# Optimization experiments

Hardware: AMD Instinct MI355X
Metric: run time of the kernel (lower is better)

The kernel has to match this reference:

```python
import jax, jax.numpy as jnp
import numpy as np

NUM_EMBEDDINGS = 1024
EMBEDDING_DIM = 256
COMMITMENT_COST = 0.02


def setup_inputs() -> dict:
    key = jax.random.key(0)
    k1, k2 = jax.random.split(key)
    z = jax.random.normal(k1, (64, 256, 32, 32), dtype=jnp.float32)
    # torch init: uniform(-1/K, 1/K)
    emb = jax.random.uniform(k2, (NUM_EMBEDDINGS, EMBEDDING_DIM), dtype=jnp.float32,
                             minval=-1.0 / NUM_EMBEDDINGS, maxval=1.0 / NUM_EMBEDDINGS)
    return {"z": z, "emb": emb}


def reference(z, emb):
    n, d, h, w = z.shape
    # (N, D, H, W) -> (N*H*W, D)
    z_flat = jnp.transpose(z, (0, 2, 3, 1)).reshape(-1, d)
    # squared L2 distances: ||z||^2 - 2 z.E^T + ||E||^2  -> (NHW, K)
    distances = (jnp.sum(z_flat * z_flat, axis=1, keepdims=True)
                 - 2.0 * z_flat @ emb.T
                 + jnp.sum(emb * emb, axis=1))
    indices = jnp.argmin(distances, axis=1)  # (NHW,)
    z_q = jnp.transpose(emb[indices].reshape(n, h, w, d), (0, 3, 1, 2))  # (N, D, H, W)
    # straight-through estimator
    z_q_st = z + jax.lax.stop_gradient(z_q - z)
    commitment_loss = COMMITMENT_COST * jnp.mean((jax.lax.stop_gradient(z) - z_q) ** 2)
    codebook_loss = jnp.mean((z - jax.lax.stop_gradient(z_q)) ** 2)
    vq_loss = commitment_loss + codebook_loss
    indices_reshaped = indices.reshape(n, h, w)
    return z_q_st, indices_reshaped, vq_loss
```

## Files before the change

### kernel.cpp

```cpp
#include <hip/hip_runtime.h>
#include <hip/hip_bf16.h>
#include <float.h>

#define OUT_IDX_OFF 16777216
#define OUT_LOSS_OFF 16842752
#define CAND_OFF 8388608
#define GMIN_OFF 12582912
#define GCNT_OFF 13107200
#define NSLOT 32
#define DELTA 2.0e-3f

typedef __attribute__((ext_vector_type(8))) short short8;
typedef __attribute__((ext_vector_type(4))) float f32x4;

static __device__ __forceinline__ unsigned short f2bf(float f) {
  union { __hip_bfloat16 h; unsigned short u; } cv;
  cv.h = __float2bfloat16(f);
  return cv.u;
}

__global__ __launch_bounds__(256) void k_prep(const float* __restrict__ emb,
                                              unsigned short* __restrict__ E2,
                                              float* __restrict__ cws) {
  const int k = blockIdx.x, d = threadIdx.x;
  const float v = emb[k * 256 + d];
  __shared__ float red[256];
  __shared__ unsigned short row[256];
  row[d] = f2bf(v);
  red[d] = v * v;
  __syncthreads();
  for (int s = 128; s > 0; s >>= 1) {
    if (d < s) red[d] += red[d + s];
    __syncthreads();
  }
  if (d == 0) cws[k] = red[0];
  if (d < 32) ((short8*)&E2[k * 256])[d] = ((short8*)row)[d];
}

__global__ __launch_bounds__(256) void k_cvt2(const float* __restrict__ z,
                                              unsigned short* __restrict__ A2) {
  __shared__ float tile[64][65];
  const int t = threadIdx.x;
  const int pt = blockIdx.x >> 2, dt = blockIdx.x & 3;
  const int p0 = pt << 6, d0 = dt << 6;
  const int n = p0 >> 10, hw0 = p0 & 1023;
  const float* zb = z + (size_t)n * 262144 + (size_t)d0 * 1024 + hw0;
  const int hwl = (t & 15) << 2;
#pragma unroll
  for (int i = 0; i < 4; ++i) {
    const int dl = (t >> 4) + i * 16;
    const float4 v = *(const float4*)&zb[(size_t)dl * 1024 + hwl];
    tile[hwl + 0][dl] = v.x;
    tile[hwl + 1][dl] = v.y;
    tile[hwl + 2][dl] = v.z;
    tile[hwl + 3][dl] = v.w;
  }
  __syncthreads();
  const int pl = t >> 2, c = t & 3;
  unsigned short* dst = &A2[(size_t)(p0 + pl) * 256 + d0];
#pragma unroll
  for (int h = 0; h < 2; ++h) {
    const int ch = c + h * 4;
    unsigned short tmp[8];
#pragma unroll
    for (int j = 0; j < 8; ++j) tmp[j] = f2bf(tile[pl][ch * 8 + j]);
    *(short8*)&dst[ch * 8] = *(short8*)tmp;
  }
}

__global__ __launch_bounds__(256) void k_a(const float* __restrict__ z,
                                           float* __restrict__ aws) {
#pragma clang fp contract(off)
  const int t = threadIdx.x;
  const int r = (blockIdx.x << 7) + (t & 127);
  const int h = t >> 7;
  const int n = r >> 10;
  const int hw = r & 1023;
  const float* zp = z + (size_t)n * 262144 + hw + (size_t)h * 131072;
  float acc[8];
#pragma unroll
  for (int j = 0; j < 8; ++j) {
    const float x = zp[(size_t)j * 1024];
    acc[j] = x * x;
  }
  for (int g = 1; g < 16; ++g) {
#pragma unroll
    for (int j = 0; j < 8; ++j) {
      const float x = zp[(size_t)(g * 8 + j) * 1024];
      const float p = x * x;
      acc[j] = acc[j] + p;
    }
  }
  const float s = ((acc[0] + acc[1]) + (acc[2] + acc[3])) +
                  ((acc[4] + acc[5]) + (acc[6] + acc[7]));
  __shared__ float red[256];
  red[t] = s;
  __syncthreads();
  if (t < 128) aws[(blockIdx.x << 7) + t] = red[t] + red[t + 128];
}

__global__ __launch_bounds__(256, 4) void k_gemm4(
    const unsigned short* __restrict__ A2, const unsigned short* __restrict__ E2,
    const float* __restrict__ cws, const float* __restrict__ aws,
    int* __restrict__ gmin, int* __restrict__ gcnt,
    float2* __restrict__ gcand) {
  __shared__ __align__(16) unsigned short As[128 * 64];
  __shared__ __align__(16) unsigned short Bs[128 * 64];
  __shared__ float a_l[128], c_l[128], rmkt[256], bmin[128];

  const int t = threadIdx.x;
  const int lane = t & 63;
  const int wave = __builtin_amdgcn_readfirstlane(t >> 6);
  const int wr = wave >> 1, wc = wave & 1;
  const int quad = lane >> 4, l15 = lane & 15;
  const int swa = l15 & 7;

  const int bid = blockIdx.x;
  const int L = ((bid & 7) << 9) + (bid >> 3);
  const int rb = L >> 3, ck = L & 7;
  const int r0 = rb << 7, k0 = ck << 7;

  if (t < 128) {
    a_l[t] = aws[r0 + t];
    c_l[t] = cws[k0 + t];
  }

  const int srow = t >> 3;
  const int gpos = t & 7;

  f32x4 acc[4][4];
#pragma unroll
  for (int a = 0; a < 4; ++a)
#pragma unroll
    for (int b = 0; b < 4; ++b) acc[a][b] = (f32x4)(0.0f);

  for (int kt = 0; kt < 4; ++kt) {
    if (kt) __syncthreads();
#pragma unroll
    for (int i = 0; i < 4; ++i) {
      const int row = (i << 5) + srow;
      const int gsrc = gpos ^ (row & 7);
      const unsigned short* sa =
          A2 + (((size_t)(r0 + row)) << 8) + (kt << 6) + (gsrc << 3);
      __builtin_amdgcn_global_load_lds(
          (const __attribute__((address_space(1))) void*)sa,
          (__attribute__((address_space(3))) void*)(As + (i << 11) +
                                                    (wave << 9)),
          16, 0, 0);
      const unsigned short* sb =
          E2 + (((size_t)(k0 + row)) << 8) + (kt << 6) + (gsrc << 3);
      __builtin_amdgcn_global_load_lds(
          (const __attribute__((address_space(1))) void*)sb,
          (__attribute__((address_space(3))) void*)(Bs + (i << 11) +
                                                    (wave << 9)),
          16, 0, 0);
    }
    __syncthreads();
#pragma unroll
    for (int ks = 0; ks < 2; ++ks) {
      short8 af[4], bf[4];
#pragma unroll
      for (int tr = 0; tr < 4; ++tr)
        af[tr] = *(const short8*)&As[(wr * 64 + tr * 16 + l15) * 64 +
                                     (((ks * 4 + quad) ^ swa) << 3)];
#pragma unroll
      for (int tc = 0; tc < 4; ++tc)
        bf[tc] = *(const short8*)&Bs[(wc * 64 + tc * 16 + l15) * 64 +
                                     (((ks * 4 + quad) ^ swa) << 3)];
#pragma unroll
      for (int tr = 0; tr < 4; ++tr)
#pragma unroll
        for (int tc = 0; tc < 4; ++tc)
          acc[tr][tc] = __builtin_amdgcn_mfma_f32_16x16x32_bf16(
              af[tr], bf[tc], acc[tr][tc], 0, 0, 0);
    }
  }

#pragma unroll
  for (int tr = 0; tr < 4; ++tr)
#pragma unroll
    for (int rg = 0; rg < 4; ++rg) {
      const int rloc = wr * 64 + tr * 16 + quad * 4 + rg;
      const float av = a_l[rloc];
      float mn = FLT_MAX;
#pragma unroll
      for (int tc = 0; tc < 4; ++tc) {
        const int cloc = wc * 64 + tc * 16 + l15;
        const float s = av + fmaf(-2.0f, acc[tr][tc][rg], c_l[cloc]);
        mn = fminf(mn, s);
      }
      mn = fminf(mn, __shfl_xor(mn, 1));
      mn = fminf(mn, __shfl_xor(mn, 2));
      mn = fminf(mn, __shfl_xor(mn, 4));
      mn = fminf(mn, __shfl_xor(mn, 8));
      if (l15 == 0) rmkt[rloc * 2 + wc] = mn;
    }
  __syncthreads();
  if (t < 128) {
    const float m = fminf(rmkt[t * 2], rmkt[t * 2 + 1]);
    const int old = atomicMin(&gmin[r0 + t], __float_as_int(m));
    bmin[t] = fminf(m, __int_as_float(old));
  }
  __syncthreads();
#pragma unroll
  for (int tr = 0; tr < 4; ++tr)
#pragma unroll
    for (int rg = 0; rg < 4; ++rg) {
      const int rloc = wr * 64 + tr * 16 + quad * 4 + rg;
      const float av = a_l[rloc];
      const float lim = bmin[rloc] + DELTA;
#pragma unroll
      for (int tc = 0; tc < 4; ++tc) {
        const int cloc = wc * 64 + tc * 16 + l15;
        const float s = av + fmaf(-2.0f, acc[tr][tc][rg], c_l[cloc]);
        if (s <= lim) {
          const int pos = atomicAdd(&gcnt[r0 + rloc], 1);
          if (pos < NSLOT)
            gcand[(size_t)(r0 + rloc) * NSLOT + pos] =
                make_float2(s, __int_as_float(k0 + cloc));
        }
      }
    }
}

__global__ __launch_bounds__(256) void k_finish(
    const float* __restrict__ z, const float* __restrict__ emb,
    const float* __restrict__ cws, const float* __restrict__ aws,
    const int* __restrict__ gmin, const int* __restrict__ gcnt,
    const float2* __restrict__ gcand, int* __restrict__ idxws,
    float* __restrict__ out) {
  const int tid = (blockIdx.x << 8) + threadIdx.x;
  const int r = tid >> 2, sub = tid & 3;
  const float lim = __int_as_float(gmin[r]) + DELTA;
  int m = gcnt[r];
  if (m > NSLOT) m = NSLOT;
  const int n = r >> 10, hw = r & 1023;
  const float* zp = z + (size_t)n * 262144 + hw;
  const float a = aws[r];
  float bestv = FLT_MAX;
  int besti = 0x7fffffff;
  for (int ci = sub; ci < m; ci += 4) {
    const float2 p = gcand[(size_t)r * NSLOT + ci];
    if (p.x > lim) continue;
    const int k = __float_as_int(p.y);
    const float* ep = emb + (size_t)k * 256;
    float dot = 0.0f;
#pragma unroll 8
    for (int d = 0; d < 256; ++d) dot = fmaf(zp[(size_t)d * 1024], ep[d], dot);
    float s = fmaf(-2.0f, dot, a);
    s = s + cws[k];
    if (s < bestv || (s == bestv && k < besti)) {
      bestv = s;
      besti = k;
    }
  }
#pragma unroll
  for (int off = 1; off < 4; off <<= 1) {
    const float ov = __shfl_xor(bestv, off);
    const int oi = __shfl_xor(besti, off);
    if (ov < bestv || (ov == bestv && oi < besti)) {
      bestv = ov;
      besti = oi;
    }
  }
  if (sub == 0) {
    idxws[r] = besti;
    out[OUT_IDX_OFF + r] = (float)besti;
  }
  float c = (sub == 0) ? bestv : 0.0f;
#pragma unroll
  for (int off = 1; off < 64; off <<= 1) c += __shfl_xor(c, off);
  if ((threadIdx.x & 63) == 0)
    atomicAdd(&out[OUT_LOSS_OFF], c * (1.02f / 16777216.0f));
}

__global__ __launch_bounds__(256) void k_out2(const float* __restrict__ emb,
                                              const int* __restrict__ idxws,
                                              float* __restrict__ out) {
  __shared__ float zq[32][257];
  __shared__ int sidx[32];
  const int t = threadIdx.x;
  const int p0 = blockIdx.x << 5;
  const int n = p0 >> 10, hw0 = p0 & 1023;
  if (t < 32) sidx[t] = idxws[p0 + t];
  __syncthreads();
#pragma unroll
  for (int it = 0; it < 8; ++it) {
    const int i = t + (it << 8);
    const int p = i >> 6;
    const int q = (i & 63) << 2;
    const float4 v = *(const float4*)&emb[(size_t)sidx[p] * 256 + q];
    zq[p][q] = v.x;
    zq[p][q + 1] = v.y;
    zq[p][q + 2] = v.z;
    zq[p][q + 3] = v.w;
  }
  __syncthreads();
  const int p = t & 31, d0 = t >> 5;
  float* ob = out + (size_t)n * 262144 + hw0 + p;
#pragma unroll
  for (int dd = 0; dd < 32; ++dd) {
    const int d = (dd << 3) + d0;
    ob[(size_t)d * 1024] = zq[p][d];
  }
}

extern "C" void kernel_launch(void* const* d_in, const int* in_sizes, int n_in,
                              void* d_out, int out_size, void* d_ws,
                              size_t ws_size, hipStream_t stream) {
  const float* z = (const float*)d_in[0];
  const float* emb = (const float*)d_in[1];
  float* out = (float*)d_out;

  unsigned short* E2 = (unsigned short*)d_ws;
  float* cws = (float*)(E2 + 262144);
  float* aws = cws + 1024;
  int* idxws = (int*)(aws + 65536);
  unsigned short* A2 = (unsigned short*)d_out;
  float2* gcand = (float2*)(out + CAND_OFF);
  int* gmin = (int*)(out + GMIN_OFF);
  int* gcnt = (int*)(out + GCNT_OFF);

  hipMemsetAsync((char*)d_out + (size_t)OUT_LOSS_OFF * 4, 0, 4, stream);
  hipMemsetAsync(gmin, 0x7f, 65536 * 4, stream);
  hipMemsetAsync(gcnt, 0, 65536 * 4, stream);

  k_prep<<<dim3(1024), dim3(256), 0, stream>>>(emb, E2, cws);
  k_cvt2<<<dim3(4096), dim3(256), 0, stream>>>(z, A2);
  k_a<<<dim3(512), dim3(256), 0, stream>>>(z, aws);
  k_gemm4<<<dim3(4096), dim3(256), 0, stream>>>(A2, E2, cws, aws, gmin, gcnt,
                                                gcand);
  k_finish<<<dim3(1024), dim3(256), 0, stream>>>(z, emb, cws, aws, gmin, gcnt,
                                                 gcand, idxws, out);
  k_out2<<<dim3(2048), dim3(256), 0, stream>>>(emb, idxws, out);
}
```

Before: 317.9 us.

## Pre-swizzle operands into MFMA fragment layout and load directly from global

The conversion kernels now write A and E in bf16 into a fragment-ordered layout that matches the MFMA register fragments, so each lane's short8 sits contiguously per wave. The GEMM kernel drops its LDS staging buffers and barriers and reads fragments straight from global memory with coalesced 16-byte loads. This removes the LDS round trip and the per-k-step syncs. The cost is that tiles shared across blocks are no longer reused through LDS, so more traffic goes to L2. Occupancy is lowered to 3 blocks per unit, which gives more registers but can expose global load latency.

```diff
diff --git a/kernel.cpp b/kernel.cpp
--- a/kernel.cpp
+++ b/kernel.cpp
@@ -19,13 +19,14 @@
   return cv.u;
 }
 
+
 __global__ __launch_bounds__(256) void k_prep(const float* __restrict__ emb,
                                               unsigned short* __restrict__ E2,
                                               float* __restrict__ cws) {
   const int k = blockIdx.x, d = threadIdx.x;
   const float v = emb[k * 256 + d];
   __shared__ float red[256];
-  __shared__ unsigned short row[256];
+  __shared__ __align__(16) unsigned short row[256];
   row[d] = f2bf(v);
   red[d] = v * v;
   __syncthreads();
@@ -34,10 +35,17 @@
     __syncthreads();
   }
   if (d == 0) cws[k] = red[0];
-  if (d < 32) ((short8*)&E2[k * 256])[d] = ((short8*)row)[d];
-}
-
-__global__ __launch_bounds__(256) void k_cvt2(const float* __restrict__ z,
+  if (d < 32) {
+    const int kt = d >> 3, ks = (d >> 2) & 1, quad = d & 3;
+    const int ck = k >> 7, wc = (k >> 6) & 1, tc = (k >> 4) & 3, l15 = k & 15;
+    const int slab = ck * 64 + kt * 16 + ks * 8 + wc * 4 + tc;
+    const int d0 = kt * 64 + ks * 32 + quad * 8;
+    *(short8*)&E2[(((size_t)slab << 6) + (quad << 4) + l15) << 3] =
+        *(const short8*)&row[d0];
+  }
+}
+
+__global__ __launch_bounds__(256) void k_cvt3(const float* __restrict__ z,
                                               unsigned short* __restrict__ A2) {
   __shared__ float tile[64][65];
   const int t = threadIdx.x;
@@ -56,15 +64,19 @@
     tile[hwl + 3][dl] = v.w;
   }
   __syncthreads();
-  const int pl = t >> 2, c = t & 3;
-  unsigned short* dst = &A2[(size_t)(p0 + pl) * 256 + d0];
+  const int rb = pt >> 1, wr = pt & 1, kt = dt;
+  const size_t base_sh = ((size_t)(rb * 64 + wr * 32 + kt * 8)) << 9;
 #pragma unroll
   for (int h = 0; h < 2; ++h) {
-    const int ch = c + h * 4;
+    const int o = t + (h << 8);
+    const int l15o = o & 15, quado = (o >> 4) & 3;
+    const int tro = (o >> 6) & 3, kso = o >> 8;
+    const int pl = tro * 16 + l15o;
+    const int dlb = kso * 32 + quado * 8;
     unsigned short tmp[8];
 #pragma unroll
-    for (int j = 0; j < 8; ++j) tmp[j] = f2bf(tile[pl][ch * 8 + j]);
-    *(short8*)&dst[ch * 8] = *(short8*)tmp;
+    for (int j = 0; j < 8; ++j) tmp[j] = f2bf(tile[pl][dlb + j]);
+    *(short8*)&A2[base_sh + ((size_t)o << 3)] = *(short8*)tmp;
   }
 }
 
@@ -99,13 +111,11 @@
   if (t < 128) aws[(blockIdx.x << 7) + t] = red[t] + red[t + 128];
 }
 
-__global__ __launch_bounds__(256, 4) void k_gemm4(
+__global__ __launch_bounds__(256, 3) void k_gemm5(
     const unsigned short* __restrict__ A2, const unsigned short* __restrict__ E2,
     const float* __restrict__ cws, const float* __restrict__ aws,
     int* __restrict__ gmin, int* __restrict__ gcnt,
     float2* __restrict__ gcand) {
-  __shared__ __align__(16) unsigned short As[128 * 64];
-  __shared__ __align__(16) unsigned short Bs[128 * 64];
   __shared__ float a_l[128], c_l[128], rmkt[256], bmin[128];
 
   const int t = threadIdx.x;
@@ -113,7 +123,6 @@
   const int wave = __builtin_amdgcn_readfirstlane(t >> 6);
   const int wr = wave >> 1, wc = wave & 1;
   const int quad = lane >> 4, l15 = lane & 15;
-  const int swa = l15 & 7;
 
   const int bid = blockIdx.x;
   const int L = ((bid & 7) << 9) + (bid >> 3);
@@ -125,8 +134,10 @@
     c_l[t] = cws[k0 + t];
   }
 
-  const int srow = t >> 3;
-  const int gpos = t & 7;
+  const short8* Ab =
+      (const short8*)(A2 + (((((size_t)(rb * 64 + wr * 32)) << 6) + lane) << 3));
+  const short8* Bb =
+      (const short8*)(E2 + (((((size_t)(ck * 64 + wc * 4)) << 6) + lane) << 3));
 
   f32x4 acc[4][4];
 #pragma unroll
@@ -134,39 +145,17 @@
 #pragma unroll
     for (int b = 0; b < 4; ++b) acc[a][b] = (f32x4)(0.0f);
 
+#pragma unroll
   for (int kt = 0; kt < 4; ++kt) {
-    if (kt) __syncthreads();
-#pragma unroll
-    for (int i = 0; i < 4; ++i) {
-      const int row = (i << 5) + srow;
-      const int gsrc = gpos ^ (row & 7);
-      const unsigned short* sa =
-          A2 + (((size_t)(r0 + row)) << 8) + (kt << 6) + (gsrc << 3);
-      __builtin_amdgcn_global_load_lds(
-          (const __attribute__((address_space(1))) void*)sa,
-          (__attribute__((address_space(3))) void*)(As + (i << 11) +
-                                                    (wave << 9)),
-          16, 0, 0);
-      const unsigned short* sb =
-          E2 + (((size_t)(k0 + row)) << 8) + (kt << 6) + (gsrc << 3);
-      __builtin_amdgcn_global_load_lds(
-          (const __attribute__((address_space(1))) void*)sb,
-          (__attribute__((address_space(3))) void*)(Bs + (i << 11) +
-                                                    (wave << 9)),
-          16, 0, 0);
-    }
-    __syncthreads();
 #pragma unroll
     for (int ks = 0; ks < 2; ++ks) {
       short8 af[4], bf[4];
 #pragma unroll
       for (int tr = 0; tr < 4; ++tr)
-        af[tr] = *(const short8*)&As[(wr * 64 + tr * 16 + l15) * 64 +
-                                     (((ks * 4 + quad) ^ swa) << 3)];
+        af[tr] = Ab[(kt * 8 + ks * 4 + tr) * 64];
 #pragma unroll
       for (int tc = 0; tc < 4; ++tc)
-        bf[tc] = *(const short8*)&Bs[(wc * 64 + tc * 16 + l15) * 64 +
-                                     (((ks * 4 + quad) ^ swa) << 3)];
+        bf[tc] = Bb[(kt * 16 + ks * 8 + tc) * 64];
 #pragma unroll
       for (int tr = 0; tr < 4; ++tr)
 #pragma unroll
@@ -175,6 +164,8 @@
               af[tr], bf[tc], acc[tr][tc], 0, 0, 0);
     }
   }
+
+  __syncthreads();
 
 #pragma unroll
   for (int tr = 0; tr < 4; ++tr)
@@ -326,9 +317,9 @@
   hipMemsetAsync(gcnt, 0, 65536 * 4, stream);
 
   k_prep<<<dim3(1024), dim3(256), 0, stream>>>(emb, E2, cws);
-  k_cvt2<<<dim3(4096), dim3(256), 0, stream>>>(z, A2);
+  k_cvt3<<<dim3(4096), dim3(256), 0, stream>>>(z, A2);
   k_a<<<dim3(512), dim3(256), 0, stream>>>(z, aws);
-  k_gemm4<<<dim3(4096), dim3(256), 0, stream>>>(A2, E2, cws, aws, gmin, gcnt,
+  k_gemm5<<<dim3(4096), dim3(256), 0, stream>>>(A2, E2, cws, aws, gmin, gcnt,
                                                 gcand);
   k_finish<<<dim3(1024), dim3(256), 0, stream>>>(z, emb, cws, aws, gmin, gcnt,
                                                  gcand, idxws, out);
```

After: 337.8 us. +6.2%, slower.

## Fuse z norm into bf16 conversion kernel and double-buffer GEMM LDS tiles

Applied to the files above, without the earlier changes.

The separate row-norm kernel is folded into the transpose/convert kernel, so z is read from global memory once instead of twice. Each block now covers all 256 channels for 64 positions and prefetches the next channel tile while converting the current one. The GEMM kernel gains double-buffered LDS stages so the global-to-LDS load of the next k-slice overlaps the MFMA work on the current one. The cost is doubled LDS use, with the occupancy hint lowered to 2 blocks per CU, and a quarter as many blocks in the convert kernel.

```diff
diff --git a/kernel.cpp b/kernel.cpp
--- a/kernel.cpp
+++ b/kernel.cpp
@@ -37,75 +37,95 @@
   if (d < 32) ((short8*)&E2[k * 256])[d] = ((short8*)row)[d];
 }
 
-__global__ __launch_bounds__(256) void k_cvt2(const float* __restrict__ z,
-                                              unsigned short* __restrict__ A2) {
+__global__ __launch_bounds__(256) void k_cvt4(const float* __restrict__ z,
+                                              unsigned short* __restrict__ A2,
+                                              float* __restrict__ aws) {
+#pragma clang fp contract(off)
   __shared__ float tile[64][65];
+  __shared__ float red2[128];
   const int t = threadIdx.x;
-  const int pt = blockIdx.x >> 2, dt = blockIdx.x & 3;
-  const int p0 = pt << 6, d0 = dt << 6;
+  const int p0 = blockIdx.x << 6;
   const int n = p0 >> 10, hw0 = p0 & 1023;
-  const float* zb = z + (size_t)n * 262144 + (size_t)d0 * 1024 + hw0;
+  const float* zb = z + (size_t)n * 262144 + hw0;
   const int hwl = (t & 15) << 2;
-#pragma unroll
-  for (int i = 0; i < 4; ++i) {
-    const int dl = (t >> 4) + i * 16;
-    const float4 v = *(const float4*)&zb[(size_t)dl * 1024 + hwl];
-    tile[hwl + 0][dl] = v.x;
-    tile[hwl + 1][dl] = v.y;
-    tile[hwl + 2][dl] = v.z;
-    tile[hwl + 3][dl] = v.w;
-  }
-  __syncthreads();
+  const int dlb = t >> 4;
+  const int row = t & 63, h = (t >> 6) & 1;
   const int pl = t >> 2, c = t & 3;
-  unsigned short* dst = &A2[(size_t)(p0 + pl) * 256 + d0];
-#pragma unroll
-  for (int h = 0; h < 2; ++h) {
-    const int ch = c + h * 4;
-    unsigned short tmp[8];
-#pragma unroll
-    for (int j = 0; j < 8; ++j) tmp[j] = f2bf(tile[pl][ch * 8 + j]);
-    *(short8*)&dst[ch * 8] = *(short8*)tmp;
-  }
-}
-
-__global__ __launch_bounds__(256) void k_a(const float* __restrict__ z,
-                                           float* __restrict__ aws) {
-#pragma clang fp contract(off)
-  const int t = threadIdx.x;
-  const int r = (blockIdx.x << 7) + (t & 127);
-  const int h = t >> 7;
-  const int n = r >> 10;
-  const int hw = r & 1023;
-  const float* zp = z + (size_t)n * 262144 + hw + (size_t)h * 131072;
+
+  float4 v[4];
+#pragma unroll
+  for (int i = 0; i < 4; ++i)
+    v[i] = *(const float4*)&zb[(size_t)(dlb + i * 16) * 1024 + hwl];
+
   float acc[8];
-#pragma unroll
-  for (int j = 0; j < 8; ++j) {
-    const float x = zp[(size_t)j * 1024];
-    acc[j] = x * x;
-  }
-  for (int g = 1; g < 16; ++g) {
-#pragma unroll
-    for (int j = 0; j < 8; ++j) {
-      const float x = zp[(size_t)(g * 8 + j) * 1024];
-      const float p = x * x;
-      acc[j] = acc[j] + p;
-    }
-  }
-  const float s = ((acc[0] + acc[1]) + (acc[2] + acc[3])) +
-                  ((acc[4] + acc[5]) + (acc[6] + acc[7]));
-  __shared__ float red[256];
-  red[t] = s;
-  __syncthreads();
-  if (t < 128) aws[(blockIdx.x << 7) + t] = red[t] + red[t + 128];
-}
-
-__global__ __launch_bounds__(256, 4) void k_gemm4(
+
+  for (int dt = 0; dt < 4; ++dt) {
+    if (dt) __syncthreads();
+#pragma unroll
+    for (int i = 0; i < 4; ++i) {
+      const int dl = dlb + i * 16;
+      tile[hwl + 0][dl] = v[i].x;
+      tile[hwl + 1][dl] = v[i].y;
+      tile[hwl + 2][dl] = v[i].z;
+      tile[hwl + 3][dl] = v[i].w;
+    }
+    __syncthreads();
+    if (dt < 3) {
+      const float* zb2 = zb + (size_t)(dt + 1) * 65536;
+#pragma unroll
+      for (int i = 0; i < 4; ++i)
+        v[i] = *(const float4*)&zb2[(size_t)(dlb + i * 16) * 1024 + hwl];
+    }
+    unsigned short* dst = &A2[(size_t)(p0 + pl) * 256 + dt * 64];
+#pragma unroll
+    for (int hh = 0; hh < 2; ++hh) {
+      const int ch = c + hh * 4;
+      unsigned short tmp[8];
+#pragma unroll
+      for (int j = 0; j < 8; ++j) tmp[j] = f2bf(tile[pl][ch * 8 + j]);
+      *(short8*)&dst[ch * 8] = *(short8*)tmp;
+    }
+    if (t < 128 && (dt >> 1) == h) {
+      if ((dt & 1) == 0) {
+#pragma unroll
+        for (int j = 0; j < 8; ++j) {
+          const float x = tile[row][j];
+          acc[j] = x * x;
+        }
+        for (int g = 1; g < 8; ++g)
+#pragma unroll
+          for (int j = 0; j < 8; ++j) {
+            const float x = tile[row][g * 8 + j];
+            const float p = x * x;
+            acc[j] = acc[j] + p;
+          }
+      } else {
+        for (int g = 8; g < 16; ++g)
+#pragma unroll
+          for (int j = 0; j < 8; ++j) {
+            const float x = tile[row][(g - 8) * 8 + j];
+            const float p = x * x;
+            acc[j] = acc[j] + p;
+          }
+      }
+    }
+  }
+  if (t < 128) {
+    const float s = ((acc[0] + acc[1]) + (acc[2] + acc[3])) +
+                    ((acc[4] + acc[5]) + (acc[6] + acc[7]));
+    red2[t] = s;
+  }
+  __syncthreads();
+  if (t < 64) aws[p0 + t] = red2[t] + red2[t + 64];
+}
+
+__global__ __launch_bounds__(256, 2) void k_gemm6(
     const unsigned short* __restrict__ A2, const unsigned short* __restrict__ E2,
     const float* __restrict__ cws, const float* __restrict__ aws,
     int* __restrict__ gmin, int* __restrict__ gcnt,
     float2* __restrict__ gcand) {
-  __shared__ __align__(16) unsigned short As[128 * 64];
-  __shared__ __align__(16) unsigned short Bs[128 * 64];
+  __shared__ __align__(16) unsigned short As[2][8192];
+  __shared__ __align__(16) unsigned short Bs[2][8192];
   __shared__ float a_l[128], c_l[128], rmkt[256], bmin[128];
 
   const int t = threadIdx.x;
@@ -134,8 +154,7 @@
 #pragma unroll
     for (int b = 0; b < 4; ++b) acc[a][b] = (f32x4)(0.0f);
 
-  for (int kt = 0; kt < 4; ++kt) {
-    if (kt) __syncthreads();
+  auto stage = [&](int kt, int buf) {
 #pragma unroll
     for (int i = 0; i < 4; ++i) {
       const int row = (i << 5) + srow;
@@ -144,28 +163,37 @@
           A2 + (((size_t)(r0 + row)) << 8) + (kt << 6) + (gsrc << 3);
       __builtin_amdgcn_global_load_lds(
           (const __attribute__((address_space(1))) void*)sa,
-          (__attribute__((address_space(3))) void*)(As + (i << 11) +
+          (__attribute__((address_space(3))) void*)(&As[buf][0] + (i << 11) +
                                                     (wave << 9)),
           16, 0, 0);
       const unsigned short* sb =
           E2 + (((size_t)(k0 + row)) << 8) + (kt << 6) + (gsrc << 3);
       __builtin_amdgcn_global_load_lds(
           (const __attribute__((address_space(1))) void*)sb,
-          (__attribute__((address_space(3))) void*)(Bs + (i << 11) +
+          (__attribute__((address_space(3))) void*)(&Bs[buf][0] + (i << 11) +
                                                     (wave << 9)),
           16, 0, 0);
     }
-    __syncthreads();
+  };
+
+  stage(0, 0);
+  __syncthreads();
+
+#pragma unroll
+  for (int kt = 0; kt < 4; ++kt) {
+    if (kt < 3) stage(kt + 1, (kt + 1) & 1);
+    const unsigned short* as = &As[kt & 1][0];
+    const unsigned short* bs = &Bs[kt & 1][0];
 #pragma unroll
     for (int ks = 0; ks < 2; ++ks) {
       short8 af[4], bf[4];
 #pragma unroll
       for (int tr = 0; tr < 4; ++tr)
-        af[tr] = *(const short8*)&As[(wr * 64 + tr * 16 + l15) * 64 +
+        af[tr] = *(const short8*)&as[(wr * 64 + tr * 16 + l15) * 64 +
                                      (((ks * 4 + quad) ^ swa) << 3)];
 #pragma unroll
       for (int tc = 0; tc < 4; ++tc)
-        bf[tc] = *(const short8*)&Bs[(wc * 64 + tc * 16 + l15) * 64 +
+        bf[tc] = *(const short8*)&bs[(wc * 64 + tc * 16 + l15) * 64 +
                                      (((ks * 4 + quad) ^ swa) << 3)];
 #pragma unroll
       for (int tr = 0; tr < 4; ++tr)
@@ -174,6 +202,7 @@
           acc[tr][tc] = __builtin_amdgcn_mfma_f32_16x16x32_bf16(
               af[tr], bf[tc], acc[tr][tc], 0, 0, 0);
     }
+    __syncthreads();
   }
 
 #pragma unroll
@@ -326,9 +355,8 @@
   hipMemsetAsync(gcnt, 0, 65536 * 4, stream);
 
   k_prep<<<dim3(1024), dim3(256), 0, stream>>>(emb, E2, cws);
-  k_cvt2<<<dim3(4096), dim3(256), 0, stream>>>(z, A2);
-  k_a<<<dim3(512), dim3(256), 0, stream>>>(z, aws);
-  k_gemm4<<<dim3(4096), dim3(256), 0, stream>>>(A2, E2, cws, aws, gmin, gcnt,
+  k_cvt4<<<dim3(1024), dim3(256), 0, stream>>>(z, A2, aws);
+  k_gemm6<<<dim3(4096), dim3(256), 0, stream>>>(A2, E2, cws, aws, gmin, gcnt,
                                                 gcand);
   k_finish<<<dim3(1024), dim3(256), 0, stream>>>(z, emb, cws, aws, gmin, gcnt,
                                                  gcand, idxws, out);
```

New measurement: 354.1 us. 1.11x slower.
